# Optimization experiments

Hardware: AMD Instinct MI355X
Metric: run time of the kernel (lower is better)

## Reference

```python
import jax, jax.numpy as jnp
import numpy as np

N_NODES = 100000
IN_F = 256
OUT_F = 256
N_EDGES = 3200000


def setup_inputs() -> dict:
    key = jax.random.key(0)
    ks = jax.random.split(key, 10)
    return {
        "mean": jax.random.normal(ks[0], (N_NODES, IN_F), dtype=jnp.float32),
        "var": jax.random.uniform(ks[1], (N_NODES, IN_F), dtype=jnp.float32),
        "W_mean": jax.random.normal(ks[2], (IN_F, OUT_F), dtype=jnp.float32) * (1.0 / np.sqrt(IN_F)),
        "b_mean": jax.random.normal(ks[3], (OUT_F,), dtype=jnp.float32) * 0.01,
        "W_var": jax.random.normal(ks[4], (IN_F, OUT_F), dtype=jnp.float32) * (1.0 / np.sqrt(IN_F)),
        "b_var": jax.random.normal(ks[5], (OUT_F,), dtype=jnp.float32) * 0.01,
        "edge_row": jax.random.randint(ks[6], (N_EDGES,), 0, N_NODES, dtype=jnp.int32),
        "edge_col": jax.random.randint(ks[7], (N_EDGES,), 0, N_NODES, dtype=jnp.int32),
        "adj0_vals": jax.random.uniform(ks[8], (N_EDGES,), dtype=jnp.float32),
        "adj1_vals": jax.random.uniform(ks[9], (N_EDGES,), dtype=jnp.float32),
    }


def _spmm(row, col, vals, x, n_nodes):
    # out[i] = sum_{e: row[e]==i} vals[e] * x[col[e]]
    gathered = x[col] * vals[:, None]  # [E, F]
    return jax.ops.segment_sum(gathered, row, num_segments=n_nodes)


def reference(mean, var, W_mean, b_mean, W_var, b_var, edge_row, edge_col, adj0_vals, adj1_vals):
    m = jnp.dot(mean, W_mean) + b_mean          # mean_conv
    v = jnp.dot(var, W_var) + b_var             # var_conv (initial=False)
    m = jax.nn.elu(m)                           # act0
    v = jax.nn.relu(v)                          # act1
    attention = jnp.exp(-v)
    m = m * attention
    v = v * attention * attention
    m = _spmm(edge_row, edge_col, adj0_vals, m, mean.shape[0])
    v = _spmm(edge_row, edge_col, adj1_vals, v, mean.shape[0])
    return (m, v)
```

## Files before the change

### kernel.cpp

```cpp
#include <hip/hip_runtime.h>
#include <hip/hip_bf16.h>
#include <stdint.h>

#define F 256
#define KSTEP 32
#define CAP 64
#define OVMAX 200000

typedef short bhalf8 __attribute__((ext_vector_type(8)));
typedef unsigned short ushort8v __attribute__((ext_vector_type(8)));
typedef float f32x4 __attribute__((ext_vector_type(4)));
typedef int i32x4 __attribute__((ext_vector_type(4)));
typedef unsigned int u32x2 __attribute__((ext_vector_type(2)));

__device__ __forceinline__ unsigned short f2b(float f) {
    union { float f; uint32_t u; } x; x.f = f;
    uint32_t u = x.u;
    return (unsigned short)((u + 0x7FFFu + ((u >> 16) & 1u)) >> 16);
}
__device__ __forceinline__ float b2f(unsigned short h) {
    union { uint32_t u; float f; } x; x.u = ((uint32_t)h) << 16;
    return x.f;
}

__global__ __launch_bounds__(256) void setup_kernel(
    const float* __restrict__ Wm, const float* __restrict__ Wv,
    unsigned short* __restrict__ Wt, int* __restrict__ count,
    int* __restrict__ ovcnt, int N)
{
    if (blockIdx.x < 98) {
        if (blockIdx.x == 0 && threadIdx.x == 0) *ovcnt = 0;
        int gi = blockIdx.x * 1024 + threadIdx.x * 4;
        #pragma unroll
        for (int q = 0; q < 4; ++q)
            if (gi + q < N) count[gi + q] = 0;
        return;
    }
    int idx = (blockIdx.x - 98) * 256 + threadIdx.x;
    int sel = idx >> 11;
    int ks  = (idx >> 8) & 7;
    int n   = idx & 255;
    const float* W = sel ? Wv : Wm;
    unsigned short* dst = Wt + ((size_t)sel * 8 * 256 * 32) + ((size_t)(ks * 256 + n) * 32);
    #pragma unroll
    for (int kk = 0; kk < 32; ++kk)
        dst[kk] = f2b(W[(ks * 32 + kk) * 256 + n]);
}

__device__ __forceinline__ void dense_tile(
    const float* __restrict__ mean, const float* __restrict__ var,
    const unsigned short* __restrict__ Wt,
    const float* __restrict__ bm, const float* __restrict__ bv,
    unsigned short* __restrict__ mv, int N, int dbid,
    unsigned short (*Asm)[40], unsigned short (*Asv)[40],
    unsigned short (*Bsm)[40], unsigned short (*Bsv)[40])
{
    const int tid  = threadIdx.x;
    const int row0 = dbid * 64;
    const int lane = tid & 63;
    const int w    = tid >> 6;
    const int wr   = w >> 2;
    const int wc   = w & 3;
    const int lr   = lane & 15;
    const int lk   = lane >> 4;

    f32x4 accm[2][4], accv[2][4];
    #pragma unroll
    for (int i = 0; i < 2; ++i)
        #pragma unroll
        for (int j = 0; j < 4; ++j) { accm[i][j] = (f32x4)0.f; accv[i][j] = (f32x4)0.f; }

    const int srow = tid >> 3;
    const int skq  = (tid & 7) * 4;
    int sgrow = row0 + srow; if (sgrow >= N) sgrow = N - 1;

    const unsigned short* WtV = Wt + (size_t)8 * 256 * 32;

    for (int ks = 0; ks < F / KSTEP; ++ks) {
        const int k0 = ks * KSTEP;
        {
            const float4 am = *(const float4*)&mean[(size_t)sgrow * F + k0 + skq];
            const float4 av = *(const float4*)&var [(size_t)sgrow * F + k0 + skq];
            ushort4 um = { f2b(am.x), f2b(am.y), f2b(am.z), f2b(am.w) };
            ushort4 uv = { f2b(av.x), f2b(av.y), f2b(av.z), f2b(av.w) };
            *(ushort4*)&Asm[srow][skq] = um;
            *(ushort4*)&Asv[srow][skq] = uv;
        }
        {
            const unsigned short* sm = Wt  + (size_t)(ks * 256) * 32;
            const unsigned short* sv = WtV + (size_t)(ks * 256) * 32;
            #pragma unroll
            for (int h = 0; h < 2; ++h) {
                int c = tid + h * 512;
                int n = c >> 2, q = c & 3;
                *(ushort8v*)&Bsm[n][q * 8] = *(const ushort8v*)(sm + (size_t)n * 32 + q * 8);
                *(ushort8v*)&Bsv[n][q * 8] = *(const ushort8v*)(sv + (size_t)n * 32 + q * 8);
            }
        }
        __syncthreads();

        bhalf8 am0 = *(const bhalf8*)&Asm[wr*32 +  0 + lr][lk*8];
        bhalf8 am1 = *(const bhalf8*)&Asm[wr*32 + 16 + lr][lk*8];
        bhalf8 av0 = *(const bhalf8*)&Asv[wr*32 +  0 + lr][lk*8];
        bhalf8 av1 = *(const bhalf8*)&Asv[wr*32 + 16 + lr][lk*8];
        #pragma unroll
        for (int ct = 0; ct < 4; ++ct) {
            bhalf8 bmf = *(const bhalf8*)&Bsm[wc*64 + ct*16 + lr][lk*8];
            bhalf8 bvf = *(const bhalf8*)&Bsv[wc*64 + ct*16 + lr][lk*8];
            accm[0][ct] = __builtin_amdgcn_mfma_f32_16x16x32_bf16(am0, bmf, accm[0][ct], 0, 0, 0);
            accm[1][ct] = __builtin_amdgcn_mfma_f32_16x16x32_bf16(am1, bmf, accm[1][ct], 0, 0, 0);
            accv[0][ct] = __builtin_amdgcn_mfma_f32_16x16x32_bf16(av0, bvf, accv[0][ct], 0, 0, 0);
            accv[1][ct] = __builtin_amdgcn_mfma_f32_16x16x32_bf16(av1, bvf, accv[1][ct], 0, 0, 0);
        }
        __syncthreads();
    }

    #pragma unroll
    for (int rt = 0; rt < 2; ++rt) {
        #pragma unroll
        for (int ct = 0; ct < 4; ++ct) {
            const int col = wc*64 + ct*16 + lr;
            const float bmc = bm[col], bvc = bv[col];
            #pragma unroll
            for (int q = 0; q < 4; ++q) {
                int grow = row0 + wr*32 + rt*16 + lk*4 + q;
                if (grow < N) {
                    float mp = accm[rt][ct][q] + bmc;
                    float vp = accv[rt][ct][q] + bvc;
                    float me = mp > 0.f ? mp : (__expf(mp) - 1.f);
                    float vr = vp > 0.f ? vp : 0.f;
                    float att = __expf(-vr);
                    mv[(size_t)grow * 512 + col]       = f2b(me * att);
                    mv[(size_t)grow * 512 + 256 + col] = f2b(vr * att * att);
                }
            }
        }
    }
}

__global__ __launch_bounds__(512) void dense_fill_bucket_kernel(
    const float* __restrict__ mean, const float* __restrict__ var,
    const unsigned short* __restrict__ Wt,
    const float* __restrict__ bm, const float* __restrict__ bv,
    unsigned short* __restrict__ mv, int N, int DB,
    const int* __restrict__ erow, const int* __restrict__ ecol,
    const float* __restrict__ a0, const float* __restrict__ a1,
    int E, int* __restrict__ count, u32x2* __restrict__ slots,
    int* __restrict__ ovcnt, i32x4* __restrict__ ovlist)
{
    __shared__ unsigned short Asm[64][40];
    __shared__ unsigned short Asv[64][40];
    __shared__ unsigned short Bsm[256][40];
    __shared__ unsigned short Bsv[256][40];

    const int g = blockIdx.x / 5;
    const int r = blockIdx.x % 5;

    if (r != 4) {
        int i = (g * 4 + r) * 512 + threadIdx.x;
        if (i < E) {
            int   rr = erow[i];
            int   c  = ecol[i];
            float v0 = a0[i];
            float v1 = a1[i];
            int pos = atomicAdd(&count[rr], 1);
            if (pos < CAP) {
                u32x2 rc;
                rc[0] = (unsigned)c;
                rc[1] = (unsigned)f2b(v0) | ((unsigned)f2b(v1) << 16);
                slots[(size_t)rr * CAP + pos] = rc;
            } else {
                int o = atomicAdd(ovcnt, 1);
                if (o < OVMAX) {
                    i32x4 rc;
                    rc[0] = rr;
                    rc[1] = c;
                    rc[2] = __float_as_int(v0);
                    rc[3] = __float_as_int(v1);
                    ovlist[o] = rc;
                }
            }
        }
        return;
    }
    if (g >= DB) return;
    dense_tile(mean, var, Wt, bm, bv, mv, N, g, Asm, Asv, Bsm, Bsv);
}

__global__ __launch_bounds__(256) void spmm_bucket_kernel(
    const int* __restrict__ count, const u32x2* __restrict__ slots,
    const unsigned short* __restrict__ mv,
    float* __restrict__ out, int N)
{
    int w    = threadIdx.x >> 6;
    int lane = threadIdx.x & 63;
    int node = blockIdx.x * 4 + w;
    if (node >= N) return;
    int cnt = count[node];
    if (cnt > CAP) cnt = CAP;

    const bool isv = lane >= 32;
    const int  fb  = (lane & 31) * 8;
    const unsigned short* base = mv + (isv ? 256 : 0) + fb;
    const int sh = isv ? 16 : 0;

    float acc[8];
    #pragma unroll
    for (int q = 0; q < 8; ++q) acc[q] = 0.f;

    const int nb  = cnt >> 3;
    const u32x2* rp  = slots + (size_t)node * CAP;
    const u32x2* rp0 = rp;

    if (nb > 0) {
        int   c[8];
        float wt[8];
        #pragma unroll
        for (int q = 0; q < 8; ++q) {
            u32x2 rc = __builtin_nontemporal_load(rp + q);
            c[q]  = (int)rc[0];
            wt[q] = b2f((unsigned short)(rc[1] >> sh));
        }
        for (int b = 0; b < nb; ++b) {
            ushort8v p[8];
            #pragma unroll
            for (int q = 0; q < 8; ++q)
                p[q] = *(const ushort8v*)(base + (size_t)c[q] * 512);
            int   cn[8];
            float wn[8];
            if (b + 1 < nb) {
                const u32x2* rn = rp + 8;
                #pragma unroll
                for (int q = 0; q < 8; ++q) {
                    u32x2 rc = __builtin_nontemporal_load(rn + q);
                    cn[q] = (int)rc[0];
                    wn[q] = b2f((unsigned short)(rc[1] >> sh));
                }
            }
            #pragma unroll
            for (int q = 0; q < 8; ++q) {
                #pragma unroll
                for (int t = 0; t < 8; ++t) acc[t] += wt[q] * b2f(p[q][t]);
            }
            #pragma unroll
            for (int q = 0; q < 8; ++q) { c[q] = cn[q]; wt[q] = wn[q]; }
            rp += 8;
        }
    }
    for (int j = nb * 8; j < cnt; ++j) {
        u32x2 rc = rp0[j];
        int   cc = (int)rc[0];
        float a  = b2f((unsigned short)(rc[1] >> sh));
        ushort8v p = *(const ushort8v*)(base + (size_t)cc * 512);
        #pragma unroll
        for (int t = 0; t < 8; ++t) acc[t] += a * b2f(p[t]);
    }

    float* obase = out + (isv ? (size_t)N * F : 0) + (size_t)node * F + fb;
    float4 o0 = { acc[0], acc[1], acc[2], acc[3] };
    float4 o1 = { acc[4], acc[5], acc[6], acc[7] };
    *(float4*)obase       = o0;
    *(float4*)(obase + 4) = o1;
}

__global__ __launch_bounds__(256) void overflow_kernel(
    const int* __restrict__ ovcnt, const i32x4* __restrict__ ovlist,
    const unsigned short* __restrict__ mv, float* __restrict__ out, int N)
{
    int nov = *ovcnt;
    if (nov > OVMAX) nov = OVMAX;
    if (nov == 0) return;
    int gw   = (blockIdx.x * 256 + threadIdx.x) >> 6;
    int nw   = (gridDim.x * 256) >> 6;
    int lane = threadIdx.x & 63;
    const bool isv = lane >= 32;
    const int  fb  = (lane & 31) * 8;
    for (int e = gw; e < nov; e += nw) {
        i32x4 rc = ovlist[e];
        int row = rc[0], c = rc[1];
        float a = __int_as_float(isv ? rc[3] : rc[2]);
        const unsigned short* p = mv + (size_t)c * 512 + (isv ? 256 : 0) + fb;
        float* ob = out + (isv ? (size_t)N * F : 0) + (size_t)row * F + fb;
        #pragma unroll
        for (int t = 0; t < 8; ++t)
            atomicAdd(&ob[t], a * b2f(p[t]));
    }
}

extern "C" void kernel_launch(void* const* d_in, const int* in_sizes, int n_in,
                              void* d_out, int out_size, void* d_ws, size_t ws_size,
                              hipStream_t stream)
{
    const float* mean = (const float*)d_in[0];
    const float* var  = (const float*)d_in[1];
    const float* Wm   = (const float*)d_in[2];
    const float* bm   = (const float*)d_in[3];
    const float* Wv   = (const float*)d_in[4];
    const float* bv   = (const float*)d_in[5];
    const int*   erow = (const int*)d_in[6];
    const int*   ecol = (const int*)d_in[7];
    const float* a0   = (const float*)d_in[8];
    const float* a1   = (const float*)d_in[9];

    const int N = in_sizes[0] / F;
    const int E = in_sizes[6];

    const int DB = (N + 63) / 64;
    const int FB = (E + 511) / 512;
    int groups = (DB > (FB + 3) / 4) ? DB : (FB + 3) / 4;
    int total  = groups * 5;

    uintptr_t p = (uintptr_t)d_ws;
    auto take = [&](size_t bytes) {
        uintptr_t r = (p + 255) & ~(uintptr_t)255;
        p = r + bytes;
        return (void*)r;
    };

    unsigned short* mv     = (unsigned short*)take((size_t)N * 512 * 2);
    u32x2*          slots  = (u32x2*)take((size_t)N * CAP * 8);
    int*            count  = (int*)take((size_t)N * 4);
    int*            ovcnt  = (int*)take(256);
    i32x4*          ovlist = (i32x4*)take((size_t)OVMAX * 16);
    unsigned short* Wt     = (unsigned short*)take((size_t)2 * 8 * 256 * 32 * 2);

    setup_kernel<<<114, 256, 0, stream>>>(Wm, Wv, Wt, count, ovcnt, N);
    dense_fill_bucket_kernel<<<total, 512, 0, stream>>>(
        mean, var, Wt, bm, bv, mv, N, DB,
        erow, ecol, a0, a1, E, count, slots, ovcnt, ovlist);
    spmm_bucket_kernel<<<(N + 3) / 4, 256, 0, stream>>>(
        count, slots, mv, (float*)d_out, N);
    overflow_kernel<<<16, 256, 0, stream>>>(ovcnt, ovlist, mv, (float*)d_out, N);
}
```

Before: 678.6 us.

## Store fp32 edge weights in 16-byte slots and process two edges per thread

Bucket slots grow from 8 bytes to 16 bytes and now hold the column plus both edge weights in full fp32, so the fill no longer rounds the weights to bf16 and the SpMM reads each weight directly. Each fill thread now handles two edges with vectorized int2/float2 loads, and the block grouping changes from 4:1 to 2:1 fill-to-dense blocks. The dense A-tile conversion uses the packed v_cvt_pk_bf16_f32 instruction. Slot traffic doubles in both the fill writes and the SpMM reads, traded for better weight accuracy and fewer conversion instructions.

```diff
diff --git a/kernel.cpp b/kernel.cpp
--- a/kernel.cpp
+++ b/kernel.cpp
@@ -21,6 +21,11 @@
 __device__ __forceinline__ float b2f(unsigned short h) {
     union { uint32_t u; float f; } x; x.u = ((uint32_t)h) << 16;
     return x.f;
+}
+__device__ __forceinline__ unsigned int cvtpk(float lo, float hi) {
+    unsigned int r;
+    asm("v_cvt_pk_bf16_f32 %0, %1, %2" : "=v"(r) : "v"(lo), "v"(hi));
+    return r;
 }
 
 __global__ __launch_bounds__(256) void setup_kernel(
@@ -81,10 +86,10 @@
         {
             const float4 am = *(const float4*)&mean[(size_t)sgrow * F + k0 + skq];
             const float4 av = *(const float4*)&var [(size_t)sgrow * F + k0 + skq];
-            ushort4 um = { f2b(am.x), f2b(am.y), f2b(am.z), f2b(am.w) };
-            ushort4 uv = { f2b(av.x), f2b(av.y), f2b(av.z), f2b(av.w) };
-            *(ushort4*)&Asm[srow][skq] = um;
-            *(ushort4*)&Asv[srow][skq] = uv;
+            u32x2 um = { cvtpk(am.x, am.y), cvtpk(am.z, am.w) };
+            u32x2 uv = { cvtpk(av.x, av.y), cvtpk(av.z, av.w) };
+            *(u32x2*)&Asm[srow][skq] = um;
+            *(u32x2*)&Asv[srow][skq] = uv;
         }
         {
             const unsigned short* sm = Wt  + (size_t)(ks * 256) * 32;
@@ -145,7 +150,7 @@
     unsigned short* __restrict__ mv, int N, int DB,
     const int* __restrict__ erow, const int* __restrict__ ecol,
     const float* __restrict__ a0, const float* __restrict__ a1,
-    int E, int* __restrict__ count, u32x2* __restrict__ slots,
+    int E, int* __restrict__ count, i32x4* __restrict__ slots,
     int* __restrict__ ovcnt, i32x4* __restrict__ ovlist)
 {
     __shared__ unsigned short Asm[64][40];
@@ -153,30 +158,63 @@
     __shared__ unsigned short Bsm[256][40];
     __shared__ unsigned short Bsv[256][40];
 
-    const int g = blockIdx.x / 5;
-    const int r = blockIdx.x % 5;
-
-    if (r != 4) {
-        int i = (g * 4 + r) * 512 + threadIdx.x;
-        if (i < E) {
-            int   rr = erow[i];
-            int   c  = ecol[i];
-            float v0 = a0[i];
-            float v1 = a1[i];
-            int pos = atomicAdd(&count[rr], 1);
+    const int g = blockIdx.x / 3;
+    const int r = blockIdx.x % 3;
+
+    if (r != 2) {
+        int i = ((g * 2 + r) * 512 + threadIdx.x) * 2;
+        if (i + 1 < E) {
+            int2   rr = *(const int2*)&erow[i];
+            int2   cc = *(const int2*)&ecol[i];
+            float2 v0 = *(const float2*)&a0[i];
+            float2 v1 = *(const float2*)&a1[i];
+            #pragma unroll
+            for (int e = 0; e < 2; ++e) {
+                int rrr = e ? rr.y : rr.x;
+                int ccc = e ? cc.y : cc.x;
+                float w0 = e ? v0.y : v0.x;
+                float w1 = e ? v1.y : v1.x;
+                int pos = atomicAdd(&count[rrr], 1);
+                if (pos < CAP) {
+                    i32x4 rc;
+                    rc[0] = ccc;
+                    rc[1] = __float_as_int(w0);
+                    rc[2] = __float_as_int(w1);
+                    rc[3] = 0;
+                    slots[(size_t)rrr * CAP + pos] = rc;
+                } else {
+                    int o = atomicAdd(ovcnt, 1);
+                    if (o < OVMAX) {
+                        i32x4 rc;
+                        rc[0] = rrr;
+                        rc[1] = ccc;
+                        rc[2] = __float_as_int(w0);
+                        rc[3] = __float_as_int(w1);
+                        ovlist[o] = rc;
+                    }
+                }
+            }
+        } else if (i < E) {
+            int   rrr = erow[i];
+            int   ccc = ecol[i];
+            float w0  = a0[i];
+            float w1  = a1[i];
+            int pos = atomicAdd(&count[rrr], 1);
             if (pos < CAP) {
-                u32x2 rc;
-                rc[0] = (unsigned)c;
-                rc[1] = (unsigned)f2b(v0) | ((unsigned)f2b(v1) << 16);
-                slots[(size_t)rr * CAP + pos] = rc;
+                i32x4 rc;
+                rc[0] = ccc;
+                rc[1] = __float_as_int(w0);
+                rc[2] = __float_as_int(w1);
+                rc[3] = 0;
+                slots[(size_t)rrr * CAP + pos] = rc;
             } else {
                 int o = atomicAdd(ovcnt, 1);
                 if (o < OVMAX) {
                     i32x4 rc;
-                    rc[0] = rr;
-                    rc[1] = c;
-                    rc[2] = __float_as_int(v0);
-                    rc[3] = __float_as_int(v1);
+                    rc[0] = rrr;
+                    rc[1] = ccc;
+                    rc[2] = __float_as_int(w0);
+                    rc[3] = __float_as_int(w1);
                     ovlist[o] = rc;
                 }
             }
@@ -188,7 +226,7 @@
 }
 
 __global__ __launch_bounds__(256) void spmm_bucket_kernel(
-    const int* __restrict__ count, const u32x2* __restrict__ slots,
+    const int* __restrict__ count, const int* __restrict__ slots,
     const unsigned short* __restrict__ mv,
     float* __restrict__ out, int N)
 {
@@ -202,24 +240,23 @@
     const bool isv = lane >= 32;
     const int  fb  = (lane & 31) * 8;
     const unsigned short* base = mv + (isv ? 256 : 0) + fb;
-    const int sh = isv ? 16 : 0;
+    const int woff = isv ? 2 : 1;
 
     float acc[8];
     #pragma unroll
     for (int q = 0; q < 8; ++q) acc[q] = 0.f;
 
     const int nb  = cnt >> 3;
-    const u32x2* rp  = slots + (size_t)node * CAP;
-    const u32x2* rp0 = rp;
+    const int* rp  = slots + (size_t)node * CAP * 4;
+    const int* rp0 = rp;
 
     if (nb > 0) {
         int   c[8];
         float wt[8];
         #pragma unroll
         for (int q = 0; q < 8; ++q) {
-            u32x2 rc = __builtin_nontemporal_load(rp + q);
-            c[q]  = (int)rc[0];
-            wt[q] = b2f((unsigned short)(rc[1] >> sh));
+            c[q]  = __builtin_nontemporal_load(rp + q * 4);
+            wt[q] = __int_as_float(__builtin_nontemporal_load(rp + q * 4 + woff));
         }
         for (int b = 0; b < nb; ++b) {
             ushort8v p[8];
@@ -229,12 +266,11 @@
             int   cn[8];
             float wn[8];
             if (b + 1 < nb) {
-                const u32x2* rn = rp + 8;
+                const int* rn = rp + 32;
                 #pragma unroll
                 for (int q = 0; q < 8; ++q) {
-                    u32x2 rc = __builtin_nontemporal_load(rn + q);
-                    cn[q] = (int)rc[0];
-                    wn[q] = b2f((unsigned short)(rc[1] >> sh));
+                    cn[q] = __builtin_nontemporal_load(rn + q * 4);
+                    wn[q] = __int_as_float(__builtin_nontemporal_load(rn + q * 4 + woff));
                 }
             }
             #pragma unroll
@@ -244,13 +280,13 @@
             }
             #pragma unroll
             for (int q = 0; q < 8; ++q) { c[q] = cn[q]; wt[q] = wn[q]; }
-            rp += 8;
+            rp += 32;
         }
     }
     for (int j = nb * 8; j < cnt; ++j) {
-        u32x2 rc = rp0[j];
-        int   cc = (int)rc[0];
-        float a  = b2f((unsigned short)(rc[1] >> sh));
+        const int* rj = rp0 + (size_t)j * 4;
+        int   cc = rj[0];
+        float a  = __int_as_float(rj[woff]);
         ushort8v p = *(const ushort8v*)(base + (size_t)cc * 512);
         #pragma unroll
         for (int t = 0; t < 8; ++t) acc[t] += a * b2f(p[t]);
@@ -306,9 +342,9 @@
     const int E = in_sizes[6];
 
     const int DB = (N + 63) / 64;
-    const int FB = (E + 511) / 512;
-    int groups = (DB > (FB + 3) / 4) ? DB : (FB + 3) / 4;
-    int total  = groups * 5;
+    const int FB = (E + 1023) / 1024;
+    int groups = (DB > (FB + 1) / 2) ? DB : (FB + 1) / 2;
+    int total  = groups * 3;
 
     uintptr_t p = (uintptr_t)d_ws;
     auto take = [&](size_t bytes) {
@@ -318,7 +354,7 @@
     };
 
     unsigned short* mv     = (unsigned short*)take((size_t)N * 512 * 2);
-    u32x2*          slots  = (u32x2*)take((size_t)N * CAP * 8);
+    i32x4*          slots  = (i32x4*)take((size_t)N * CAP * 16);
     int*            count  = (int*)take((size_t)N * 4);
     int*            ovcnt  = (int*)take(256);
     i32x4*          ovlist = (i32x4*)take((size_t)OVMAX * 16);
@@ -329,6 +365,6 @@
         mean, var, Wt, bm, bv, mv, N, DB,
         erow, ecol, a0, a1, E, count, slots, ovcnt, ovlist);
     spmm_bucket_kernel<<<(N + 3) / 4, 256, 0, stream>>>(
-        count, slots, mv, (float*)d_out, N);
+        count, (const int*)slots, mv, (float*)d_out, N);
     overflow_kernel<<<16, 256, 0, stream>>>(ovcnt, ovlist, mv, (float*)d_out, N);
 }
```

Measured after the change: 657.7 us. 1.03x faster.
